# Optimization experiments

Measured on AMD Instinct MI355X. Metric: run time of the kernel, lower is better.

## Reference

```python
import jax, jax.numpy as jnp
import numpy as np

NUM_NODES = 100000
NUM_EDGES = 1600000
INPUT_DIM = 128
NUM_LAYERS = 3
EPS = 1e-12


def setup_inputs() -> dict:
    key = jax.random.key(0)
    k1, k2, k3, k4, k5 = jax.random.split(key, 5)
    emb = jax.random.normal(k1, (NUM_NODES, INPUT_DIM), dtype=jnp.float32)
    edge_index = jax.random.randint(k2, (2, NUM_EDGES), 0, NUM_NODES, dtype=jnp.int64)
    senders = jax.random.randint(k3, (16384,), 0, NUM_NODES, dtype=jnp.int64)
    receivers = jax.random.randint(k4, (16384,), 0, NUM_NODES, dtype=jnp.int64)
    mlp_dim = INPUT_DIM * (NUM_LAYERS + 1)  # concat aggregation -> 512
    W = jax.random.normal(k5, (mlp_dim, mlp_dim), dtype=jnp.float32) * 0.02
    b = jnp.zeros((mlp_dim,), dtype=jnp.float32)
    return {"emb": emb, "edge_index": edge_index, "senders": senders,
            "receivers": receivers, "W": W, "b": b}


def _l2_normalize(x):
    # matches F.normalize(x, p=2, dim=-1) with eps=1e-12
    n = jnp.linalg.norm(x, axis=-1, keepdims=True)
    return x / jnp.maximum(n, EPS)


def reference(emb, edge_index, senders, receivers, W, b):
    src, dst = edge_index[0], edge_index[1]
    # LightGCN-style symmetric degree normalization: 1/sqrt(d_src * d_dst)
    ones = jnp.ones((src.shape[0],), dtype=emb.dtype)
    deg = jax.ops.segment_sum(ones, dst, num_segments=NUM_NODES)
    deg = jnp.maximum(deg, 1.0)
    dinv = jax.lax.rsqrt(deg)
    norm = dinv[src] * dinv[dst]  # [E]

    x = emb
    z = [_l2_normalize(x)]
    for _ in range(NUM_LAYERS):
        msgs = x[src] * norm[:, None]                      # [E, D] gather + scale
        x = jax.ops.segment_sum(msgs, dst, num_segments=NUM_NODES)  # scatter-add
        z.append(_l2_normalize(x))
    x = jnp.concatenate(z, axis=-1)        # [N, D*(L+1)]
    x = x @ W.T + b                        # post_mlp
    return (x[senders], x[receivers])
```

## Files before the change

### kernel.cpp

```cpp
#include <hip/hip_runtime.h>

#define NN 100000
#define NE 1600000
#define DD 128
#define MD 512
#define SEL 16384
#define MROWS 32768
#define NBKT 196
#define TILE 4096
#define SEGCAP 16384

typedef __attribute__((ext_vector_type(8))) short bf16x8;
typedef __attribute__((ext_vector_type(4))) float f32x4;

__device__ __forceinline__ unsigned short f2bf(float f) {
  unsigned u = __float_as_uint(f);
  u += 0x7fff + ((u >> 16) & 1);
  return (unsigned short)(u >> 16);
}
__device__ __forceinline__ float bflo(unsigned v) { return __uint_as_float(v << 16); }
__device__ __forceinline__ float bfhi(unsigned v) { return __uint_as_float(v & 0xffff0000u); }

__global__ __launch_bounds__(256) void k_binA(const int* __restrict__ src,
                                              const int* __restrict__ dst,
                                              int* __restrict__ gcursor,
                                              unsigned* __restrict__ ebuf) {
  __shared__ int hist[NBKT];
  __shared__ int base[NBKT];
  __shared__ int cnt2[NBKT];
  const int tid = threadIdx.x;
  const long e0 = (long)blockIdx.x * TILE;
  for (int i = tid; i < NBKT; i += 256) { hist[i] = 0; cnt2[i] = 0; }
  __syncthreads();
  unsigned pk[16]; int bk[16];
  #pragma unroll
  for (int k = 0; k < 16; ++k) {
    const long e = e0 + k * 256 + tid;
    bk[k] = -1;
    if (e < NE) {
      const int d = dst[e], s = src[e];
      bk[k] = d >> 9;
      pk[k] = ((unsigned)s << 9) | (unsigned)(d & 511);
      atomicAdd(&hist[bk[k]], 1);
    }
  }
  __syncthreads();
  for (int i = tid; i < NBKT; i += 256)
    base[i] = i * SEGCAP + atomicAdd(&gcursor[i], hist[i]);
  __syncthreads();
  #pragma unroll
  for (int k = 0; k < 16; ++k) {
    if (bk[k] >= 0) {
      const int lp = atomicAdd(&cnt2[bk[k]], 1);
      ebuf[base[bk[k]] + lp] = pk[k];
    }
  }
}

__global__ __launch_bounds__(256) void k_degB(const unsigned* __restrict__ ebuf,
                                              const int* __restrict__ bcnt,
                                              int* __restrict__ deg,
                                              float* __restrict__ dinv,
                                              int* __restrict__ excl,
                                              int* __restrict__ btot,
                                              unsigned short* __restrict__ x0,
                                              unsigned short* __restrict__ x1,
                                              unsigned short* __restrict__ x2) {
  __shared__ int ld[512];
  __shared__ int ps[256];
  const int b = blockIdx.x;
  const int n0 = b << 9;
  const int nn = min(512, NN - n0);
  const int tid = threadIdx.x;
  for (int i = tid; i < 512; i += 256) ld[i] = 0;
  __syncthreads();
  const int s0 = b * SEGCAP;
  const int c = bcnt[b];
  for (int i = tid; i < c; i += 256) atomicAdd(&ld[ebuf[s0 + i] & 511], 1);
  __syncthreads();
  const int d0 = (tid * 2 < nn) ? ld[tid * 2] : 0;
  const int d1 = (tid * 2 + 1 < nn) ? ld[tid * 2 + 1] : 0;
  const int p0 = (d0 + 7) & ~7, p1 = (d1 + 7) & ~7;
  ps[tid] = p0 + p1;
  __syncthreads();
  for (int o = 1; o < 256; o <<= 1) {
    int t2 = (tid >= o) ? ps[tid - o] : 0;
    __syncthreads();
    ps[tid] += t2;
    __syncthreads();
  }
  const int exbase = ps[tid] - (p0 + p1);
  if (tid * 2 < nn) {
    deg[n0 + tid * 2] = d0;
    dinv[n0 + tid * 2] = rsqrtf(fmaxf((float)d0, 1.f));
    excl[n0 + tid * 2] = exbase;
  }
  if (tid * 2 + 1 < nn) {
    deg[n0 + tid * 2 + 1] = d1;
    dinv[n0 + tid * 2 + 1] = rsqrtf(fmaxf((float)d1, 1.f));
    excl[n0 + tid * 2 + 1] = exbase + p0;
  }
  if (tid == 255) btot[b] = ps[255];
  if (b == 0 && tid < 64) {
    ((unsigned*)(x0 + (size_t)NN * DD))[tid] = 0u;
    ((unsigned*)(x1 + (size_t)NN * DD))[tid] = 0u;
    ((unsigned*)(x2 + (size_t)NN * DD))[tid] = 0u;
  }
}

__global__ __launch_bounds__(256) void k_binB(const unsigned* __restrict__ ebuf,
                                              const int* __restrict__ bcnt,
                                              const int* __restrict__ btot,
                                              const int* __restrict__ excl,
                                              int* __restrict__ rowstart,
                                              int* __restrict__ csr) {
  __shared__ int seg[SEGCAP];
  __shared__ int rs[512];
  __shared__ int cnt[512];
  __shared__ int sm[256];
  const int b = blockIdx.x;
  const int n0 = b << 9;
  const int nn = min(512, NN - n0);
  const int tid = threadIdx.x;
  int v = (tid < NBKT) ? btot[tid] : 0;
  sm[tid] = v;
  __syncthreads();
  for (int o = 1; o < 256; o <<= 1) {
    int t2 = (tid >= o) ? sm[tid - o] : 0;
    __syncthreads();
    sm[tid] += t2;
    __syncthreads();
  }
  const int seg0 = b ? sm[b - 1] : 0;
  const int seglen = btot[b];
  for (int i = tid; i < nn; i += 256) {
    const int ex = excl[n0 + i];
    rs[i] = ex;
    cnt[i] = 0;
    rowstart[n0 + i] = seg0 + ex;
  }
  for (int i = tid; i < seglen; i += 256) seg[i] = NN;
  __syncthreads();
  const int s0 = b * SEGCAP;
  const int c = bcnt[b];
  for (int i = tid; i < c; i += 256) {
    const unsigned e = ebuf[s0 + i];
    const int dl = e & 511;
    const int pos = rs[dl] + atomicAdd(&cnt[dl], 1);
    seg[pos] = (int)(e >> 9);
  }
  __syncthreads();
  for (int i = tid; i < seglen; i += 256) csr[seg0 + i] = seg[i];
}

__global__ void k_mark(const int* __restrict__ sl, const int* __restrict__ rl,
                       int* __restrict__ mark) {
  int i = blockIdx.x * blockDim.x + threadIdx.x;
  if (i < SEL) mark[sl[i]] = 1;
  else if (i < 2 * SEL) mark[rl[i - SEL]] = 1;
}

__global__ void k_compact(const int* __restrict__ mark, int* __restrict__ list,
                          int* __restrict__ cnt, int* __restrict__ uidx) {
  int n = blockIdx.x * blockDim.x + threadIdx.x;
  if (n < NN && mark[n]) {
    int p = atomicAdd(cnt, 1);
    list[p] = n;
    uidx[n] = p;
  }
}

template<int WX>
__global__ __launch_bounds__(256) void k_aggf(const int* __restrict__ rowstart,
                                              const int* __restrict__ deg,
                                              const int* __restrict__ csr,
                                              const float* __restrict__ dinv,
                                              const unsigned short* __restrict__ xin,
                                              unsigned short* __restrict__ xout,
                                              unsigned short* __restrict__ zbuf,
                                              const int* __restrict__ uidx,
                                              int zcol,
                                              const int* __restrict__ list,
                                              const int* __restrict__ lcnt) {
  const int lane = threadIdx.x & 63;
  const int wid = (blockIdx.x * blockDim.x + threadIdx.x) >> 6;
  const int nw = (gridDim.x * blockDim.x) >> 6;
  const int total = WX ? NN : *lcnt;
  for (int it = wid; it < total; it += nw) {
    const int n = WX ? it : list[it];
    const int start = rowstart[n];
    const int cntp = (deg[n] + 7) & ~7;
    float ax[8], ay[8];
    #pragma unroll
    for (int u = 0; u < 8; ++u) { ax[u] = 0.f; ay[u] = 0.f; }
    for (int j = 0; j < cntp; j += 8) {
      const int4 e0 = *(const int4*)(csr + start + j);
      const int4 e1 = *(const int4*)(csr + start + j + 4);
      unsigned v[8];
      v[0] = ((const unsigned*)(xin + (size_t)e0.x * DD))[lane];
      v[1] = ((const unsigned*)(xin + (size_t)e0.y * DD))[lane];
      v[2] = ((const unsigned*)(xin + (size_t)e0.z * DD))[lane];
      v[3] = ((const unsigned*)(xin + (size_t)e0.w * DD))[lane];
      v[4] = ((const unsigned*)(xin + (size_t)e1.x * DD))[lane];
      v[5] = ((const unsigned*)(xin + (size_t)e1.y * DD))[lane];
      v[6] = ((const unsigned*)(xin + (size_t)e1.z * DD))[lane];
      v[7] = ((const unsigned*)(xin + (size_t)e1.w * DD))[lane];
      #pragma unroll
      for (int u = 0; u < 8; ++u) { ax[u] += bflo(v[u]); ay[u] += bfhi(v[u]); }
    }
    const float s = dinv[n] * dinv[n];
    const float rx = (((ax[0] + ax[1]) + (ax[2] + ax[3])) + ((ax[4] + ax[5]) + (ax[6] + ax[7]))) * s;
    const float ry = (((ay[0] + ay[1]) + (ay[2] + ay[3])) + ((ay[4] + ay[5]) + (ay[6] + ay[7]))) * s;
    if (WX)
      ((unsigned*)(xout + (size_t)n * DD))[lane] = ((unsigned)f2bf(ry) << 16) | f2bf(rx);
    const int uz = uidx[n];
    if (uz >= 0) {
      float ss = fmaf(rx, rx, ry * ry);
      #pragma unroll
      for (int m = 32; m >= 1; m >>= 1) ss += __shfl_xor(ss, m);
      const float sc = 1.0f / fmaxf(sqrtf(ss), 1e-12f);
      *(unsigned*)(zbuf + (size_t)uz * MD + zcol + lane * 2) =
          ((unsigned)f2bf(ry * sc) << 16) | f2bf(rx * sc);
    }
  }
}

__global__ __launch_bounds__(256) void k_conv_emb2(const float* __restrict__ emb,
                                                   const float* __restrict__ dinv,
                                                   const int* __restrict__ uidx,
                                                   unsigned short* __restrict__ x0,
                                                   unsigned short* __restrict__ zbuf,
                                                   const float* __restrict__ W,
                                                   unsigned short* __restrict__ Wbf) {
  if (blockIdx.x >= NN / 4) {
    const int i = (blockIdx.x - NN / 4) * 256 + threadIdx.x;
    if (i < MD * MD / 4) {
      float4 v = ((const float4*)W)[i];
      ushort4 o;
      o.x = f2bf(v.x); o.y = f2bf(v.y); o.z = f2bf(v.z); o.w = f2bf(v.w);
      ((ushort4*)Wbf)[i] = o;
    }
    return;
  }
  const int lane = threadIdx.x & 63;
  const int n = blockIdx.x * 4 + (threadIdx.x >> 6);
  const float2 v = ((const float2*)(emb + (size_t)n * DD))[lane];
  const float d = dinv[n];
  *(unsigned*)(x0 + (size_t)n * DD + lane * 2) =
      ((unsigned)f2bf(v.y * d) << 16) | f2bf(v.x * d);
  const int uz = uidx[n];
  if (uz >= 0) {
    float ss = fmaf(v.x, v.x, v.y * v.y);
    #pragma unroll
    for (int m = 32; m >= 1; m >>= 1) ss += __shfl_xor(ss, m);
    const float sc = 1.0f / fmaxf(sqrtf(ss), 1e-12f);
    *(unsigned*)(zbuf + (size_t)uz * MD + lane * 2) =
        ((unsigned)f2bf(v.y * sc) << 16) | f2bf(v.x * sc);
  }
}

__global__ __launch_bounds__(256) void k_gemm(const unsigned short* __restrict__ zbuf,
                                              const int* __restrict__ sl,
                                              const int* __restrict__ rl,
                                              const int* __restrict__ uidx,
                                              const unsigned short* __restrict__ B,
                                              const float* __restrict__ bias,
                                              float* __restrict__ out) {
  __shared__ __align__(16) char smraw[20480];
  unsigned short (*As)[40] = (unsigned short(*)[40])smraw;
  unsigned short (*Bs)[40] = (unsigned short(*)[40])(smraw + 10240);
  float (*et)[132] = (float(*)[132])smraw;
  const int t = threadIdx.x;
  const int bid = blockIdx.x;
  const int xcd = bid & 7;
  const int j = bid >> 3;
  const int mt = xcd * 32 + (j >> 2);
  const int nt = j & 3;
  const int i0 = mt * 128, j0 = nt * 128;
  const int lane = t & 63, wid = t >> 6;
  const int wr = wid >> 1, wc = wid & 1;
  const int fr = lane & 15, kg = lane >> 4;
  const int srow = t >> 2, seg = t & 3;
  const int r0 = i0 + srow, r1 = r0 + 64;
  const int nd0 = (r0 < SEL) ? sl[r0] : rl[r0 - SEL];
  const int nd1 = (r1 < SEL) ? sl[r1] : rl[r1 - SEL];
  const unsigned short* pa0 = zbuf + (size_t)uidx[nd0] * MD + seg * 8;
  const unsigned short* pa1 = zbuf + (size_t)uidx[nd1] * MD + seg * 8;
  const unsigned short* pb0 = B + (size_t)(j0 + srow) * MD + seg * 8;
  const unsigned short* pb1 = B + (size_t)(j0 + srow + 64) * MD + seg * 8;
  f32x4 acc[4][4] = {};
  for (int k0 = 0; k0 < MD; k0 += 32) {
    *(float4*)(&As[srow][seg * 8]) = *(const float4*)(pa0 + k0);
    *(float4*)(&As[srow + 64][seg * 8]) = *(const float4*)(pa1 + k0);
    *(float4*)(&Bs[srow][seg * 8]) = *(const float4*)(pb0 + k0);
    *(float4*)(&Bs[srow + 64][seg * 8]) = *(const float4*)(pb1 + k0);
    __syncthreads();
    bf16x8 af[4], bfr[4];
    #pragma unroll
    for (int m = 0; m < 4; ++m)
      af[m] = *(const bf16x8*)(&As[wr * 64 + m * 16 + fr][kg * 8]);
    #pragma unroll
    for (int n = 0; n < 4; ++n)
      bfr[n] = *(const bf16x8*)(&Bs[wc * 64 + n * 16 + fr][kg * 8]);
    #pragma unroll
    for (int m = 0; m < 4; ++m)
      #pragma unroll
      for (int n = 0; n < 4; ++n)
        acc[m][n] = __builtin_amdgcn_mfma_f32_16x16x32_bf16(af[m], bfr[n], acc[m][n], 0, 0, 0);
    __syncthreads();
  }
  #pragma unroll
  for (int m = 0; m < 4; ++m) {
    __syncthreads();
    #pragma unroll
    for (int n = 0; n < 4; ++n)
      #pragma unroll
      for (int r = 0; r < 4; ++r)
        et[wr * 16 + kg * 4 + r][wc * 64 + n * 16 + fr] = acc[m][n][r];
    __syncthreads();
    #pragma unroll
    for (int w = 0; w < 4; ++w) {
      const int idx = w * 256 + t;
      const int lrow = idx >> 5, lc4 = idx & 31;
      const int grow = i0 + (lrow >> 4) * 64 + m * 16 + (lrow & 15);
      const int gcol = j0 + lc4 * 4;
      const float4 bv = *(const float4*)(bias + gcol);
      float4 o;
      o.x = et[lrow][lc4 * 4 + 0] + bv.x;
      o.y = et[lrow][lc4 * 4 + 1] + bv.y;
      o.z = et[lrow][lc4 * 4 + 2] + bv.z;
      o.w = et[lrow][lc4 * 4 + 3] + bv.w;
      *(float4*)(out + (size_t)grow * MD + gcol) = o;
    }
  }
}

extern "C" void kernel_launch(void* const* d_in, const int* in_sizes, int n_in,
                              void* d_out, int out_size, void* d_ws, size_t ws_size,
                              hipStream_t stream) {
  const float* emb = (const float*)d_in[0];
  const int* ei = (const int*)d_in[1];
  const int* esrc = ei;
  const int* edst = ei + NE;
  const int* send = (const int*)d_in[2];
  const int* recv = (const int*)d_in[3];
  const float* W = (const float*)d_in[4];
  const float* bias = (const float*)d_in[5];
  float* out = (float*)d_out;

  char* ws = (char*)d_ws;
  size_t off = 0;
  auto take = [&](size_t b) {
    char* p = ws + off;
    off = (off + b + 1023) & ~(size_t)1023;
    return p;
  };
  const size_t CSRN = (size_t)NE + 8 * (size_t)NN;
  int* zblk = (int*)take((size_t)(NBKT + 1 + NN) * 4);
  int* gcursor = zblk;
  int* lcnt = zblk + NBKT;
  int* mark = zblk + NBKT + 1;
  int* uidx = (int*)take((size_t)NN * 4);
  float* dinv = (float*)take((size_t)NN * 4);
  int* degI = (int*)take((size_t)NN * 4);
  int* rowstart = (int*)take((size_t)NN * 4);
  int* excl = (int*)take((size_t)NN * 4);
  int* btot = (int*)take(NBKT * 4);
  int* list = (int*)take((size_t)MROWS * 4);
  unsigned* ebuf = (unsigned*)take((size_t)NBKT * SEGCAP * 4);
  int* csr = (int*)take(CSRN * 4);
  unsigned short* x0 = (unsigned short*)take((size_t)(NN + 1) * DD * 2);
  unsigned short* x1 = (unsigned short*)take((size_t)(NN + 1) * DD * 2);
  unsigned short* x2 = (unsigned short*)take((size_t)(NN + 1) * DD * 2);
  unsigned short* zbuf = (unsigned short*)take((size_t)MROWS * MD * 2);
  unsigned short* Wbf = (unsigned short*)take((size_t)MD * MD * 2);
  (void)ws_size; (void)in_sizes; (void)n_in; (void)out_size;

  hipMemsetAsync(zblk, 0, (size_t)(NBKT + 1 + NN) * 4, stream);
  hipMemsetAsync(uidx, 0xFF, (size_t)NN * 4, stream);

  k_binA<<<(NE + TILE - 1) / TILE, 256, 0, stream>>>(esrc, edst, gcursor, ebuf);
  k_degB<<<NBKT, 256, 0, stream>>>(ebuf, gcursor, degI, dinv, excl, btot, x0, x1, x2);
  k_binB<<<NBKT, 256, 0, stream>>>(ebuf, gcursor, btot, excl, rowstart, csr);

  k_mark<<<(2 * SEL + 255) / 256, 256, 0, stream>>>(send, recv, mark);
  k_compact<<<(NN + 255) / 256, 256, 0, stream>>>(mark, list, lcnt, uidx);
  k_conv_emb2<<<NN / 4 + MD * MD / 4 / 256, 256, 0, stream>>>(emb, dinv, uidx, x0,
                                                              zbuf, W, Wbf);

  k_aggf<1><<<2048, 256, 0, stream>>>(rowstart, degI, csr, dinv, x0, x1,
                                      zbuf, uidx, 128, list, lcnt);
  k_aggf<1><<<2048, 256, 0, stream>>>(rowstart, degI, csr, dinv, x1, x2,
                                      zbuf, uidx, 256, list, lcnt);
  k_aggf<0><<<1024, 256, 0, stream>>>(rowstart, degI, csr, dinv, x2, x0,
                                      zbuf, uidx, 384, list, lcnt);

  k_gemm<<<(MROWS / 128) * (MD / 128), 256, 0, stream>>>(zbuf, send, recv, uidx,
                                                         Wbf, bias, out);
}
```

Before: 289.0 us.

## Split feature halves across XCDs in aggregation and move normalization to separate pass

The aggregation kernel now has each wave handle two nodes at once, each half-wave gathering 64 of the 128 features. Which half a block handles is chosen from the XCD-interleaved block ID, so each XCD's L2 only has to cache half of every gathered row. The L2-normalization and zbuf writes are removed from the aggregation and embedding conversion kernels and done in a new k_zall pass over the selected nodes. The last layer writes only the selected rows into a compact buffer. The cost is an extra kernel launch, re-reading x0, x1 and x2 for the selected rows, and reliance on blocks being assigned to XCDs round-robin.

```diff
diff --git a/kernel.cpp b/kernel.cpp
--- a/kernel.cpp
+++ b/kernel.cpp
@@ -171,25 +171,30 @@
 }
 
 template<int WX>
-__global__ __launch_bounds__(256) void k_aggf(const int* __restrict__ rowstart,
+__global__ __launch_bounds__(256) void k_aggs(const int* __restrict__ rowstart,
                                               const int* __restrict__ deg,
                                               const int* __restrict__ csr,
                                               const float* __restrict__ dinv,
                                               const unsigned short* __restrict__ xin,
                                               unsigned short* __restrict__ xout,
-                                              unsigned short* __restrict__ zbuf,
-                                              const int* __restrict__ uidx,
-                                              int zcol,
                                               const int* __restrict__ list,
                                               const int* __restrict__ lcnt) {
   const int lane = threadIdx.x & 63;
-  const int wid = (blockIdx.x * blockDim.x + threadIdx.x) >> 6;
-  const int nw = (gridDim.x * blockDim.x) >> 6;
+  const int hi = lane >> 5, l5 = lane & 31;
+  const int bid = blockIdx.x;
+  const int xcd = bid & 7;
+  const int h = xcd >> 2;
+  const int g = (bid >> 3) * 4 + (xcd & 3);
+  const int wvh = g * 4 + (threadIdx.x >> 6);
+  const int stride = gridDim.x * 2;
+  const int xoff = h * 64;
   const int total = WX ? NN : *lcnt;
-  for (int it = wid; it < total; it += nw) {
-    const int n = WX ? it : list[it];
+  for (int p = wvh; 2 * p < total; p += stride) {
+    const int idx = 2 * p + hi;
+    const bool act = idx < total;
+    const int n = act ? (WX ? idx : list[idx]) : 0;
     const int start = rowstart[n];
-    const int cntp = (deg[n] + 7) & ~7;
+    const int cntp = act ? ((deg[n] + 7) & ~7) : 0;
     float ax[8], ay[8];
     #pragma unroll
     for (int u = 0; u < 8; ++u) { ax[u] = 0.f; ay[u] = 0.f; }
@@ -197,39 +202,62 @@
       const int4 e0 = *(const int4*)(csr + start + j);
       const int4 e1 = *(const int4*)(csr + start + j + 4);
       unsigned v[8];
-      v[0] = ((const unsigned*)(xin + (size_t)e0.x * DD))[lane];
-      v[1] = ((const unsigned*)(xin + (size_t)e0.y * DD))[lane];
-      v[2] = ((const unsigned*)(xin + (size_t)e0.z * DD))[lane];
-      v[3] = ((const unsigned*)(xin + (size_t)e0.w * DD))[lane];
-      v[4] = ((const unsigned*)(xin + (size_t)e1.x * DD))[lane];
-      v[5] = ((const unsigned*)(xin + (size_t)e1.y * DD))[lane];
-      v[6] = ((const unsigned*)(xin + (size_t)e1.z * DD))[lane];
-      v[7] = ((const unsigned*)(xin + (size_t)e1.w * DD))[lane];
+      v[0] = ((const unsigned*)(xin + (size_t)e0.x * DD + xoff))[l5];
+      v[1] = ((const unsigned*)(xin + (size_t)e0.y * DD + xoff))[l5];
+      v[2] = ((const unsigned*)(xin + (size_t)e0.z * DD + xoff))[l5];
+      v[3] = ((const unsigned*)(xin + (size_t)e0.w * DD + xoff))[l5];
+      v[4] = ((const unsigned*)(xin + (size_t)e1.x * DD + xoff))[l5];
+      v[5] = ((const unsigned*)(xin + (size_t)e1.y * DD + xoff))[l5];
+      v[6] = ((const unsigned*)(xin + (size_t)e1.z * DD + xoff))[l5];
+      v[7] = ((const unsigned*)(xin + (size_t)e1.w * DD + xoff))[l5];
       #pragma unroll
       for (int u = 0; u < 8; ++u) { ax[u] += bflo(v[u]); ay[u] += bfhi(v[u]); }
     }
-    const float s = dinv[n] * dinv[n];
-    const float rx = (((ax[0] + ax[1]) + (ax[2] + ax[3])) + ((ax[4] + ax[5]) + (ax[6] + ax[7]))) * s;
-    const float ry = (((ay[0] + ay[1]) + (ay[2] + ay[3])) + ((ay[4] + ay[5]) + (ay[6] + ay[7]))) * s;
-    if (WX)
-      ((unsigned*)(xout + (size_t)n * DD))[lane] = ((unsigned)f2bf(ry) << 16) | f2bf(rx);
-    const int uz = uidx[n];
-    if (uz >= 0) {
-      float ss = fmaf(rx, rx, ry * ry);
+    if (act) {
+      const float s = dinv[n] * dinv[n];
+      const float rx = (((ax[0] + ax[1]) + (ax[2] + ax[3])) + ((ax[4] + ax[5]) + (ax[6] + ax[7]))) * s;
+      const float ry = (((ay[0] + ay[1]) + (ay[2] + ay[3])) + ((ay[4] + ay[5]) + (ay[6] + ay[7]))) * s;
+      const size_t orow = WX ? (size_t)n : (size_t)idx;
+      ((unsigned*)(xout + orow * DD + xoff))[l5] =
+          ((unsigned)f2bf(ry) << 16) | f2bf(rx);
+    }
+  }
+}
+
+__global__ __launch_bounds__(256) void k_zall(const int* __restrict__ list,
+                                              const int* __restrict__ lcnt,
+                                              const unsigned short* __restrict__ x0,
+                                              const unsigned short* __restrict__ x1,
+                                              const unsigned short* __restrict__ x2,
+                                              const unsigned short* __restrict__ u3c,
+                                              unsigned short* __restrict__ zbuf) {
+  const int lane = threadIdx.x & 63;
+  const int wv = (blockIdx.x * blockDim.x + threadIdx.x) >> 6;
+  const int nw = (gridDim.x * blockDim.x) >> 6;
+  const int cl = *lcnt;
+  for (int r = wv; r < cl; r += nw) {
+    const int node = list[r];
+    unsigned v[4];
+    v[0] = ((const unsigned*)(x0 + (size_t)node * DD))[lane];
+    v[1] = ((const unsigned*)(x1 + (size_t)node * DD))[lane];
+    v[2] = ((const unsigned*)(x2 + (size_t)node * DD))[lane];
+    v[3] = ((const unsigned*)(u3c + (size_t)r * DD))[lane];
+    #pragma unroll
+    for (int q = 0; q < 4; ++q) {
+      const float a = bflo(v[q]), b = bfhi(v[q]);
+      float ss = fmaf(a, a, b * b);
       #pragma unroll
       for (int m = 32; m >= 1; m >>= 1) ss += __shfl_xor(ss, m);
       const float sc = 1.0f / fmaxf(sqrtf(ss), 1e-12f);
-      *(unsigned*)(zbuf + (size_t)uz * MD + zcol + lane * 2) =
-          ((unsigned)f2bf(ry * sc) << 16) | f2bf(rx * sc);
+      *(unsigned*)(zbuf + (size_t)r * MD + q * DD + lane * 2) =
+          ((unsigned)f2bf(b * sc) << 16) | f2bf(a * sc);
     }
   }
 }
 
 __global__ __launch_bounds__(256) void k_conv_emb2(const float* __restrict__ emb,
                                                    const float* __restrict__ dinv,
-                                                   const int* __restrict__ uidx,
                                                    unsigned short* __restrict__ x0,
-                                                   unsigned short* __restrict__ zbuf,
                                                    const float* __restrict__ W,
                                                    unsigned short* __restrict__ Wbf) {
   if (blockIdx.x >= NN / 4) {
@@ -248,15 +276,6 @@
   const float d = dinv[n];
   *(unsigned*)(x0 + (size_t)n * DD + lane * 2) =
       ((unsigned)f2bf(v.y * d) << 16) | f2bf(v.x * d);
-  const int uz = uidx[n];
-  if (uz >= 0) {
-    float ss = fmaf(v.x, v.x, v.y * v.y);
-    #pragma unroll
-    for (int m = 32; m >= 1; m >>= 1) ss += __shfl_xor(ss, m);
-    const float sc = 1.0f / fmaxf(sqrtf(ss), 1e-12f);
-    *(unsigned*)(zbuf + (size_t)uz * MD + lane * 2) =
-        ((unsigned)f2bf(v.y * sc) << 16) | f2bf(v.x * sc);
-  }
 }
 
 __global__ __launch_bounds__(256) void k_gemm(const unsigned short* __restrict__ zbuf,
@@ -372,6 +391,7 @@
   unsigned short* x0 = (unsigned short*)take((size_t)(NN + 1) * DD * 2);
   unsigned short* x1 = (unsigned short*)take((size_t)(NN + 1) * DD * 2);
   unsigned short* x2 = (unsigned short*)take((size_t)(NN + 1) * DD * 2);
+  unsigned short* u3c = (unsigned short*)take((size_t)MROWS * DD * 2);
   unsigned short* zbuf = (unsigned short*)take((size_t)MROWS * MD * 2);
   unsigned short* Wbf = (unsigned short*)take((size_t)MD * MD * 2);
   (void)ws_size; (void)in_sizes; (void)n_in; (void)out_size;
@@ -385,16 +405,13 @@
 
   k_mark<<<(2 * SEL + 255) / 256, 256, 0, stream>>>(send, recv, mark);
   k_compact<<<(NN + 255) / 256, 256, 0, stream>>>(mark, list, lcnt, uidx);
-  k_conv_emb2<<<NN / 4 + MD * MD / 4 / 256, 256, 0, stream>>>(emb, dinv, uidx, x0,
-                                                              zbuf, W, Wbf);
-
-  k_aggf<1><<<2048, 256, 0, stream>>>(rowstart, degI, csr, dinv, x0, x1,
-                                      zbuf, uidx, 128, list, lcnt);
-  k_aggf<1><<<2048, 256, 0, stream>>>(rowstart, degI, csr, dinv, x1, x2,
-                                      zbuf, uidx, 256, list, lcnt);
-  k_aggf<0><<<1024, 256, 0, stream>>>(rowstart, degI, csr, dinv, x2, x0,
-                                      zbuf, uidx, 384, list, lcnt);
-
+  k_conv_emb2<<<NN / 4 + MD * MD / 4 / 256, 256, 0, stream>>>(emb, dinv, x0, W, Wbf);
+
+  k_aggs<1><<<2048, 256, 0, stream>>>(rowstart, degI, csr, dinv, x0, x1, list, lcnt);
+  k_aggs<1><<<2048, 256, 0, stream>>>(rowstart, degI, csr, dinv, x1, x2, list, lcnt);
+  k_aggs<0><<<1024, 256, 0, stream>>>(rowstart, degI, csr, dinv, x2, u3c, list, lcnt);
+
+  k_zall<<<1024, 256, 0, stream>>>(list, lcnt, x0, x1, x2, u3c, zbuf);
   k_gemm<<<(MROWS / 128) * (MD / 128), 256, 0, stream>>>(zbuf, send, recv, uidx,
                                                          Wbf, bias, out);
 }
```

New measurement: 287.9 us. About the same (-0.4%).
